# Kernel optimization log

Measured on AMD Instinct MI355X. Metric: run time of the kernel, lower is better.

The kernel has to match this reference:

```python
import jax, jax.numpy as jnp
import numpy as np

EPS = 1e-12

def setup_inputs() -> dict:
    key = jax.random.key(0)
    k1, k2, k3, k4, k5, k6 = jax.random.split(key, 6)
    B, DIM, T = 16, 256, 2048
    K, D = 1024, 64  # num_embeddings, embedding_dim
    N = B * T
    input_data = jax.random.normal(k1, (B, DIM, T), dtype=jnp.float32)
    codebooks = jax.random.normal(k2, (K, D), dtype=jnp.float32)
    W_in = jax.random.normal(k3, (DIM, D), dtype=jnp.float32) / np.sqrt(DIM)
    b_in = jnp.zeros((D,), dtype=jnp.float32)
    W_out = jax.random.normal(k4, (D, DIM), dtype=jnp.float32) / np.sqrt(D)
    b_out = jnp.zeros((DIM,), dtype=jnp.float32)
    random_vector = jax.random.normal(k5, (N, D), dtype=jnp.float32)
    return {"input_data": input_data, "codebooks": codebooks,
            "W_in": W_in, "b_in": b_in, "W_out": W_out, "b_out": b_out,
            "random_vector": random_vector}

def reference(input_data, codebooks, W_in, b_in, W_out, b_out, random_vector):
    B, DIM, T = input_data.shape
    D = codebooks.shape[1]
    # encode: [B, DIM, T] -> [B, T, DIM] -> project -> [B*T, D]
    x = jnp.einsum('bct,cd->btd', input_data, W_in) + b_in
    x = x.reshape(-1, D)  # [N, D]
    distances = (jnp.sum(x * x, axis=1, keepdims=True)
                 - 2.0 * (x @ codebooks.T)
                 + jnp.sum(codebooks * codebooks, axis=1)[None, :])  # [N, K]
    min_indices = jnp.argmin(distances, axis=1)  # [N]
    hard = codebooks[min_indices]  # [N, D]
    # noise substitution
    norm_resid = jnp.sqrt(jnp.sum((x - hard) ** 2, axis=1, keepdims=True))
    norm_rand = jnp.sqrt(jnp.sum(random_vector ** 2, axis=1, keepdims=True))
    vq_error = (norm_resid / (norm_rand + EPS)) * random_vector
    q = x + vq_error  # [N, D]
    # decode: [N, D] -> [B, T, D] -> project_out -> [B, DIM, T]
    q = q.reshape(B, T, D)
    out = jnp.einsum('btd,dc->bct', q, W_out) + b_out[None, :, None]
    return out
```

## Files before the change

kernel.cpp:

```cpp
#include <hip/hip_runtime.h>
#include <hip/hip_bf16.h>

typedef __bf16 bf16x8 __attribute__((ext_vector_type(8)));
typedef unsigned short u16x8 __attribute__((ext_vector_type(8)));
typedef unsigned short u16x4 __attribute__((ext_vector_type(4)));
typedef float f32x4 __attribute__((ext_vector_type(4)));
typedef unsigned short u16;

constexpr int DIMc = 256, Tt = 2048, Kk = 1024, Dd = 64;

#define WS_WINT 0
#define WS_CBX  18432
#define WS_WOX  116736

__device__ __forceinline__ u16 f2b(float f) {
  unsigned u = __float_as_uint(f);
  return (u16)((u + 0x7FFFu + ((u >> 16) & 1u)) >> 16);
}
__device__ __forceinline__ float b2f(u16 v) {
  return __uint_as_float(((unsigned)v) << 16);
}
__device__ __forceinline__ f32x4 mfma16(u16x8 a, u16x8 b, f32x4 c) {
  return __builtin_amdgcn_mfma_f32_16x16x32_bf16(
      __builtin_bit_cast(bf16x8, a), __builtin_bit_cast(bf16x8, b), c, 0, 0, 0);
}
__device__ __forceinline__ void dma16(const u16* g, u16* l) {
  __builtin_amdgcn_global_load_lds(
      (const __attribute__((address_space(1))) unsigned int*)g,
      (__attribute__((address_space(3))) unsigned int*)l, 16, 0, 0);
}

__global__ void nsvq_prep(const float* __restrict__ cb, const float* __restrict__ Win,
                          const float* __restrict__ bin, const float* __restrict__ Wout,
                          const float* __restrict__ bout, u16* __restrict__ wsu) {
  const int g = blockIdx.x * 256 + threadIdx.x;
  u16* WinT = wsu + WS_WINT;
  u16* CbX  = wsu + WS_CBX;
  u16* WoX  = wsu + WS_WOX;
  for (int i = g; i < 16384; i += 8192) {
    int c = i >> 6, d = i & 63;
    WinT[d * 288 + c] = f2b(Win[i]);
  }
  if (g < 2048) {
    int d = g >> 5, j = g & 31; u16 v = 0;
    float bv = bin[d]; u16 h = f2b(bv);
    if (j == 0) v = h; else if (j == 1) v = f2b(bv - b2f(h));
    WinT[d * 288 + 256 + j] = v;
  }
  if (g < 1024) {
    const float4* cr = (const float4*)(cb + (size_t)g * 64);
    float vb[64]; float cn = 0.f;
    #pragma unroll
    for (int q = 0; q < 16; ++q) {
      float4 v = cr[q];
      vb[q*4] = v.x; vb[q*4+1] = v.y; vb[q*4+2] = v.z; vb[q*4+3] = v.w;
      cn = fmaf(v.x, v.x, fmaf(v.y, v.y, fmaf(v.z, v.z, fmaf(v.w, v.w, cn))));
    }
    u16* row = CbX + g * 96;
    #pragma unroll
    for (int d = 0; d < 64; ++d) row[d] = f2b(-2.f * vb[d]);
    u16 h = f2b(cn);
    row[64] = h; row[65] = f2b(cn - b2f(h));
    for (int j = 66; j < 96; ++j) row[j] = 0;
  }
  for (int i = g; i < 16384; i += 8192) {
    int d = i >> 8, c = i & 255;
    WoX[c * 96 + d] = f2b(Wout[i]);
  }
  {
    int c = g >> 5, j = g & 31; u16 v = 0;
    float bv = bout[c]; u16 h = f2b(bv);
    if (j == 0) v = h; else if (j == 1) v = f2b(bv - b2f(h));
    WoX[c * 96 + 64 + j] = v;
  }
}

__global__ __launch_bounds__(512, 2) void nsvq_main(
    const float* __restrict__ in, const float* __restrict__ rnd,
    const u16* __restrict__ wsu, float* __restrict__ out) {
  __shared__ u16 buf[24576];
  __shared__ u16 InT[128 * 256];
  __shared__ u16 Xt[128 * 64];
  __shared__ float mnp[8][128];

  const int tid = threadIdx.x;
  const int lane = tid & 63;
  const int w = tid >> 6;
  const int quad = lane >> 4, col = lane & 15;
  const int b  = blockIdx.x >> 4;
  const int t0 = (blockIdx.x & 15) << 7;
  const int myt = w * 16 + col;

  {
    const int t = tid & 127, cg = tid >> 7;
    const float* ib = in + (size_t)b * DIMc * Tt + t0 + t;
    #pragma unroll
    for (int it = 0; it < 8; ++it) {
      int c0 = cg * 8 + it * 32;
      u16x8 pk;
      #pragma unroll
      for (int j = 0; j < 8; ++j) pk[j] = f2b(ib[(size_t)(c0 + j) * Tt]);
      *(u16x8*)(InT + t * 256 + ((((c0 >> 3)) ^ (t & 7)) << 3)) = pk;
    }
  }
  #pragma unroll
  for (int ii = 0; ii < 5; ++ii) {
    int i = w + 8 * ii;
    if (i < 36) dma16(wsu + WS_WINT + i * 512 + lane * 8, buf + i * 512);
  }
  float rr2v = 0.f;
  const float* rb = rnd + ((size_t)b * Tt + t0) * Dd;
  #pragma unroll
  for (int tt = 0; tt < 16; ++tt) {
    float v = rb[(size_t)(w * 16 + tt) * Dd + lane];
    float s = v * v;
    s += __shfl_xor(s, 1);  s += __shfl_xor(s, 2);  s += __shfl_xor(s, 4);
    s += __shfl_xor(s, 8);  s += __shfl_xor(s, 16); s += __shfl_xor(s, 32);
    if (col == tt) rr2v = s;
  }
  __syncthreads();

  u16x8 Bc1 = {0, 0, 0, 0, 0, 0, 0, 0};
  if (quad == 0) { Bc1[0] = 0x3F80; Bc1[1] = 0x3F80; }
  f32x4 acc[4];
  {
    u16x8 Bf[8];
    #pragma unroll
    for (int kt = 0; kt < 8; ++kt)
      Bf[kt] = *(const u16x8*)(InT + myt * 256 + (((kt * 4 + quad) ^ (myt & 7)) << 3));
    #pragma unroll
    for (int mt = 0; mt < 4; ++mt) {
      f32x4 a = {0.f, 0.f, 0.f, 0.f};
      #pragma unroll
      for (int kt = 0; kt < 8; ++kt) {
        u16x8 A = *(const u16x8*)(buf + (mt * 16 + col) * 288 + kt * 32 + quad * 8);
        a = mfma16(A, Bf[kt], a);
      }
      u16x8 A8 = *(const u16x8*)(buf + (mt * 16 + col) * 288 + 256 + quad * 8);
      acc[mt] = mfma16(A8, Bc1, a);
    }
  }
  float x2v = 0.f;
  #pragma unroll
  for (int mt = 0; mt < 4; ++mt) {
    u16x4 pk;
    #pragma unroll
    for (int r = 0; r < 4; ++r) { x2v = fmaf(acc[mt][r], acc[mt][r], x2v); pk[r] = f2b(acc[mt][r]); }
    int bk = mt * 2 + (quad >> 1);
    *(u16x4*)(Xt + myt * 64 + ((bk ^ (myt & 7)) << 3) + (quad & 1) * 4) = pk;
  }
  x2v += __shfl_xor(x2v, 16);
  x2v += __shfl_xor(x2v, 32);
  __syncthreads();

  u16x8 Xa[8], Xb[8];
  #pragma unroll
  for (int nt = 0; nt < 8; ++nt) {
    int tr = nt * 16 + col;
    Xa[nt] = *(const u16x8*)(Xt + tr * 64 + ((quad ^ (tr & 7)) << 3));
    Xb[nt] = *(const u16x8*)(Xt + tr * 64 + (((4 + quad) ^ (tr & 7)) << 3));
  }
  float minv[8];
  #pragma unroll
  for (int i = 0; i < 8; ++i) minv[i] = 3.4e38f;
  for (int ch = 0; ch < 4; ++ch) {
    if (ch) __syncthreads();
    #pragma unroll
    for (int ii = 0; ii < 6; ++ii) {
      int i = w + 8 * ii;
      dma16(wsu + WS_CBX + ch * 24576 + i * 512 + lane * 8, buf + i * 512);
    }
    __syncthreads();
    #pragma unroll
    for (int ms = 0; ms < 2; ++ms) {
      const u16* ar = buf + (w * 32 + ms * 16 + col) * 96;
      u16x8 A0 = *(const u16x8*)(ar + quad * 8);
      u16x8 A1 = *(const u16x8*)(ar + 32 + quad * 8);
      u16x8 A2 = *(const u16x8*)(ar + 64 + quad * 8);
      #pragma unroll
      for (int nt = 0; nt < 8; ++nt) {
        f32x4 a = {0.f, 0.f, 0.f, 0.f};
        a = mfma16(A0, Xa[nt], a);
        a = mfma16(A1, Xb[nt], a);
        a = mfma16(A2, Bc1, a);
        #pragma unroll
        for (int r = 0; r < 4; ++r) minv[nt] = fminf(minv[nt], a[r]);
      }
    }
  }
  #pragma unroll
  for (int nt = 0; nt < 8; ++nt) {
    float m = minv[nt];
    m = fminf(m, __shfl_xor(m, 16));
    m = fminf(m, __shfl_xor(m, 32));
    mnp[w][nt * 16 + col] = m;
  }
  __syncthreads();

  #pragma unroll
  for (int ii = 0; ii < 6; ++ii) {
    int i = w + 8 * ii;
    dma16(wsu + WS_WOX + i * 512 + lane * 8, buf + i * 512);
  }
  float mv = 3.4e38f;
  #pragma unroll
  for (int j = 0; j < 8; ++j) mv = fminf(mv, mnp[j][myt]);
  float r2  = fmaxf(x2v + mv, 0.f);
  float scv = sqrtf(r2) / (sqrtf(rr2v) + 1e-12f);
  #pragma unroll
  for (int tt = 0; tt < 16; ++tt) {
    float s = __shfl(scv, tt);
    float rv = rb[(size_t)(w * 16 + tt) * Dd + lane];
    int tr = w * 16 + tt;
    int idx = tr * 64 + (((lane >> 3) ^ (tr & 7)) << 3) + (lane & 7);
    Xt[idx] = f2b(fmaf(s, rv, b2f(Xt[idx])));
  }
  __syncthreads();

  u16x8 Q0 = *(const u16x8*)(Xt + myt * 64 + ((quad ^ (myt & 7)) << 3));
  u16x8 Q1 = *(const u16x8*)(Xt + myt * 64 + (((4 + quad) ^ (myt & 7)) << 3));
  float* ob0 = out + (size_t)b * DIMc * Tt + t0 + myt;
  #pragma unroll
  for (int mt = 0; mt < 16; ++mt) {
    const u16* ar = buf + (mt * 16 + col) * 96;
    u16x8 A0 = *(const u16x8*)(ar + quad * 8);
    u16x8 A1 = *(const u16x8*)(ar + 32 + quad * 8);
    u16x8 A2 = *(const u16x8*)(ar + 64 + quad * 8);
    f32x4 a = {0.f, 0.f, 0.f, 0.f};
    a = mfma16(A0, Q0, a);
    a = mfma16(A1, Q1, a);
    a = mfma16(A2, Bc1, a);
    float* ob = ob0 + (size_t)(mt * 16 + quad * 4) * Tt;
    #pragma unroll
    for (int r = 0; r < 4; ++r) ob[(size_t)r * Tt] = a[r];
  }
}

extern "C" void kernel_launch(void* const* d_in, const int* in_sizes, int n_in,
                              void* d_out, int out_size, void* d_ws, size_t ws_size,
                              hipStream_t stream) {
  const float *in = nullptr, *cb = nullptr, *rnd = nullptr, *bin = nullptr, *bout = nullptr;
  const float* w16[2] = {nullptr, nullptr}; int nw = 0;
  for (int i = 0; i < n_in; ++i) {
    switch (in_sizes[i]) {
      case 8388608: in  = (const float*)d_in[i]; break;
      case 65536:   cb  = (const float*)d_in[i]; break;
      case 2097152: rnd = (const float*)d_in[i]; break;
      case 64:      bin = (const float*)d_in[i]; break;
      case 256:     bout= (const float*)d_in[i]; break;
      case 16384:   if (nw < 2) w16[nw++] = (const float*)d_in[i]; break;
      default: break;
    }
  }
  if (!in)  in  = (const float*)d_in[0];
  if (!cb)  cb  = (const float*)d_in[1];
  if (nw < 2) { w16[0] = (const float*)d_in[2]; w16[1] = (const float*)d_in[4]; }
  if (!bin) bin = (const float*)d_in[3];
  if (!bout) bout = (const float*)d_in[5];
  if (!rnd) rnd = (const float*)d_in[6];

  u16* wsu = (u16*)d_ws;
  float* outp = (float*)d_out;

  nsvq_prep<<<32, 256, 0, stream>>>(cb, w16[0], bin, w16[1], bout, wsu);
  nsvq_main<<<256, 512, 0, stream>>>(in, rnd, wsu, outp);
}
```

Baseline: 116.3 us.

## Fuse weight prep into main kernel and stream codebook from global

Removes the separate prep kernel and workspace. Each block now converts W_in and W_out to bf16 into shared memory itself, and reads codebook rows straight from global memory into MFMA operands, computing the codebook norms on the fly. The -2 scale moves onto a second copy of x kept in shared memory. Biases and codebook norms are now fed as MFMA accumulator initial values instead of extra MFMAs with split bf16 hi/lo terms, which trades away that hi/lo precision trick. This saves one launch and the per-chunk LDS staging and barriers, at the cost of redundant weight conversion in every block, more global codebook traffic per block, and a larger shared-memory footprint.

```diff
diff --git a/kernel.cpp b/kernel.cpp
--- a/kernel.cpp
+++ b/kernel.cpp
@@ -3,15 +3,12 @@
 
 typedef __bf16 bf16x8 __attribute__((ext_vector_type(8)));
 typedef unsigned short u16x8 __attribute__((ext_vector_type(8)));
-typedef unsigned short u16x4 __attribute__((ext_vector_type(4)));
+typedef unsigned int u32x2 __attribute__((ext_vector_type(2)));
+typedef unsigned int u32x4 __attribute__((ext_vector_type(4)));
 typedef float f32x4 __attribute__((ext_vector_type(4)));
 typedef unsigned short u16;
 
-constexpr int DIMc = 256, Tt = 2048, Kk = 1024, Dd = 64;
-
-#define WS_WINT 0
-#define WS_CBX  18432
-#define WS_WOX  116736
+constexpr int DIMc = 256, Tt = 2048, Dd = 64;
 
 __device__ __forceinline__ u16 f2b(float f) {
   unsigned u = __float_as_uint(f);
@@ -20,93 +17,61 @@
 __device__ __forceinline__ float b2f(u16 v) {
   return __uint_as_float(((unsigned)v) << 16);
 }
+__device__ __forceinline__ unsigned f2b2(float a, float b) {
+  return (unsigned)f2b(a) | ((unsigned)f2b(b) << 16);
+}
 __device__ __forceinline__ f32x4 mfma16(u16x8 a, u16x8 b, f32x4 c) {
   return __builtin_amdgcn_mfma_f32_16x16x32_bf16(
       __builtin_bit_cast(bf16x8, a), __builtin_bit_cast(bf16x8, b), c, 0, 0, 0);
 }
-__device__ __forceinline__ void dma16(const u16* g, u16* l) {
-  __builtin_amdgcn_global_load_lds(
-      (const __attribute__((address_space(1))) unsigned int*)g,
-      (__attribute__((address_space(3))) unsigned int*)l, 16, 0, 0);
-}
-
-__global__ void nsvq_prep(const float* __restrict__ cb, const float* __restrict__ Win,
-                          const float* __restrict__ bin, const float* __restrict__ Wout,
-                          const float* __restrict__ bout, u16* __restrict__ wsu) {
-  const int g = blockIdx.x * 256 + threadIdx.x;
-  u16* WinT = wsu + WS_WINT;
-  u16* CbX  = wsu + WS_CBX;
-  u16* WoX  = wsu + WS_WOX;
-  for (int i = g; i < 16384; i += 8192) {
-    int c = i >> 6, d = i & 63;
-    WinT[d * 288 + c] = f2b(Win[i]);
-  }
-  if (g < 2048) {
-    int d = g >> 5, j = g & 31; u16 v = 0;
-    float bv = bin[d]; u16 h = f2b(bv);
-    if (j == 0) v = h; else if (j == 1) v = f2b(bv - b2f(h));
-    WinT[d * 288 + 256 + j] = v;
-  }
-  if (g < 1024) {
-    const float4* cr = (const float4*)(cb + (size_t)g * 64);
-    float vb[64]; float cn = 0.f;
-    #pragma unroll
-    for (int q = 0; q < 16; ++q) {
-      float4 v = cr[q];
-      vb[q*4] = v.x; vb[q*4+1] = v.y; vb[q*4+2] = v.z; vb[q*4+3] = v.w;
-      cn = fmaf(v.x, v.x, fmaf(v.y, v.y, fmaf(v.z, v.z, fmaf(v.w, v.w, cn))));
-    }
-    u16* row = CbX + g * 96;
-    #pragma unroll
-    for (int d = 0; d < 64; ++d) row[d] = f2b(-2.f * vb[d]);
-    u16 h = f2b(cn);
-    row[64] = h; row[65] = f2b(cn - b2f(h));
-    for (int j = 66; j < 96; ++j) row[j] = 0;
-  }
-  for (int i = g; i < 16384; i += 8192) {
-    int d = i >> 8, c = i & 255;
-    WoX[c * 96 + d] = f2b(Wout[i]);
-  }
-  {
-    int c = g >> 5, j = g & 31; u16 v = 0;
-    float bv = bout[c]; u16 h = f2b(bv);
-    if (j == 0) v = h; else if (j == 1) v = f2b(bv - b2f(h));
-    WoX[c * 96 + 64 + j] = v;
-  }
-}
-
-__global__ __launch_bounds__(512, 2) void nsvq_main(
+
+__global__ __launch_bounds__(512, 2) void nsvq_fused(
     const float* __restrict__ in, const float* __restrict__ rnd,
-    const u16* __restrict__ wsu, float* __restrict__ out) {
-  __shared__ u16 buf[24576];
-  __shared__ u16 InT[128 * 256];
-  __shared__ u16 Xt[128 * 64];
-  __shared__ float mnp[8][128];
-
-  const int tid = threadIdx.x;
+    const float* __restrict__ cb, const float* __restrict__ Win,
+    const float* __restrict__ bin, const float* __restrict__ Wout,
+    const float* __restrict__ bout, float* __restrict__ out) {
+  __shared__ u16 sm[69632];
+  u16* const WinT = sm;
+  u16* const InT  = sm + 18432;
+  u16* const WoX  = sm + 18432;
+  u16* const Xt   = sm + 51200;
+  u16* const Xm   = sm + 59392;
+  float* const mnp = (float*)(sm + 67584);
+
+  const int tid  = threadIdx.x;
   const int lane = tid & 63;
-  const int w = tid >> 6;
+  const int w    = tid >> 6;
   const int quad = lane >> 4, col = lane & 15;
-  const int b  = blockIdx.x >> 4;
-  const int t0 = (blockIdx.x & 15) << 7;
-  const int myt = w * 16 + col;
-
+  const int b    = blockIdx.x >> 4;
+  const int t0   = (blockIdx.x & 15) << 7;
+  const int myt  = w * 16 + col;
+
+  {
+    const int c = tid & 255, db = tid >> 8;
+    #pragma unroll
+    for (int k = 0; k < 4; ++k) {
+      const int d0 = db * 32 + k * 8;
+      const float4* wr = (const float4*)(Win + c * 64 + d0);
+      float4 v0 = wr[0], v1 = wr[1];
+      u16* dst = WinT + c;
+      dst[(d0 + 0) * 288] = f2b(v0.x); dst[(d0 + 1) * 288] = f2b(v0.y);
+      dst[(d0 + 2) * 288] = f2b(v0.z); dst[(d0 + 3) * 288] = f2b(v0.w);
+      dst[(d0 + 4) * 288] = f2b(v1.x); dst[(d0 + 5) * 288] = f2b(v1.y);
+      dst[(d0 + 6) * 288] = f2b(v1.z); dst[(d0 + 7) * 288] = f2b(v1.w);
+    }
+  }
   {
     const int t = tid & 127, cg = tid >> 7;
     const float* ib = in + (size_t)b * DIMc * Tt + t0 + t;
     #pragma unroll
     for (int it = 0; it < 8; ++it) {
-      int c0 = cg * 8 + it * 32;
-      u16x8 pk;
-      #pragma unroll
-      for (int j = 0; j < 8; ++j) pk[j] = f2b(ib[(size_t)(c0 + j) * Tt]);
-      *(u16x8*)(InT + t * 256 + ((((c0 >> 3)) ^ (t & 7)) << 3)) = pk;
-    }
-  }
-  #pragma unroll
-  for (int ii = 0; ii < 5; ++ii) {
-    int i = w + 8 * ii;
-    if (i < 36) dma16(wsu + WS_WINT + i * 512 + lane * 8, buf + i * 512);
+      const int c0 = cg * 8 + it * 32;
+      u32x4 pk;
+      #pragma unroll
+      for (int jj = 0; jj < 4; ++jj)
+        pk[jj] = f2b2(ib[(size_t)(c0 + 2 * jj) * Tt], ib[(size_t)(c0 + 2 * jj + 1) * Tt]);
+      *(u32x4*)(InT + t * 256 + (((c0 >> 3) ^ (t & 7)) << 3)) = pk;
+    }
   }
   float rr2v = 0.f;
   const float* rb = rnd + ((size_t)b * Tt + t0) * Dd;
@@ -120,8 +85,6 @@
   }
   __syncthreads();
 
-  u16x8 Bc1 = {0, 0, 0, 0, 0, 0, 0, 0};
-  if (quad == 0) { Bc1[0] = 0x3F80; Bc1[1] = 0x3F80; }
   f32x4 acc[4];
   {
     u16x8 Bf[8];
@@ -130,62 +93,80 @@
       Bf[kt] = *(const u16x8*)(InT + myt * 256 + (((kt * 4 + quad) ^ (myt & 7)) << 3));
     #pragma unroll
     for (int mt = 0; mt < 4; ++mt) {
-      f32x4 a = {0.f, 0.f, 0.f, 0.f};
+      float4 bi = *(const float4*)(bin + mt * 16 + quad * 4);
+      f32x4 a = {bi.x, bi.y, bi.z, bi.w};
       #pragma unroll
       for (int kt = 0; kt < 8; ++kt) {
-        u16x8 A = *(const u16x8*)(buf + (mt * 16 + col) * 288 + kt * 32 + quad * 8);
+        u16x8 A = *(const u16x8*)(WinT + (mt * 16 + col) * 288 + kt * 32 + quad * 8);
         a = mfma16(A, Bf[kt], a);
       }
-      u16x8 A8 = *(const u16x8*)(buf + (mt * 16 + col) * 288 + 256 + quad * 8);
-      acc[mt] = mfma16(A8, Bc1, a);
+      acc[mt] = a;
     }
   }
   float x2v = 0.f;
   #pragma unroll
   for (int mt = 0; mt < 4; ++mt) {
-    u16x4 pk;
-    #pragma unroll
-    for (int r = 0; r < 4; ++r) { x2v = fmaf(acc[mt][r], acc[mt][r], x2v); pk[r] = f2b(acc[mt][r]); }
-    int bk = mt * 2 + (quad >> 1);
-    *(u16x4*)(Xt + myt * 64 + ((bk ^ (myt & 7)) << 3) + (quad & 1) * 4) = pk;
+    #pragma unroll
+    for (int r = 0; r < 4; ++r) x2v = fmaf(acc[mt][r], acc[mt][r], x2v);
+    u32x2 px = { f2b2(acc[mt][0], acc[mt][1]), f2b2(acc[mt][2], acc[mt][3]) };
+    u32x2 pm = { f2b2(-2.f * acc[mt][0], -2.f * acc[mt][1]),
+                 f2b2(-2.f * acc[mt][2], -2.f * acc[mt][3]) };
+    const int bk  = mt * 2 + (quad >> 1);
+    const int off = myt * 64 + ((bk ^ (myt & 7)) << 3) + (quad & 1) * 4;
+    *(u32x2*)(Xt + off) = px;
+    *(u32x2*)(Xm + off) = pm;
   }
   x2v += __shfl_xor(x2v, 16);
   x2v += __shfl_xor(x2v, 32);
   __syncthreads();
 
+  {
+    const int c = tid & 255, db = tid >> 8;
+    #pragma unroll
+    for (int k = 0; k < 4; ++k) {
+      const int d0 = db * 32 + k * 8;
+      u32x4 pk;
+      #pragma unroll
+      for (int jj = 0; jj < 4; ++jj)
+        pk[jj] = f2b2(Wout[(size_t)(d0 + 2 * jj) * 256 + c],
+                      Wout[(size_t)(d0 + 2 * jj + 1) * 256 + c]);
+      *(u32x4*)(WoX + c * 72 + d0) = pk;
+    }
+  }
   u16x8 Xa[8], Xb[8];
   #pragma unroll
   for (int nt = 0; nt < 8; ++nt) {
-    int tr = nt * 16 + col;
-    Xa[nt] = *(const u16x8*)(Xt + tr * 64 + ((quad ^ (tr & 7)) << 3));
-    Xb[nt] = *(const u16x8*)(Xt + tr * 64 + (((4 + quad) ^ (tr & 7)) << 3));
+    const int tr = nt * 16 + col;
+    Xa[nt] = *(const u16x8*)(Xm + tr * 64 + ((quad ^ (tr & 7)) << 3));
+    Xb[nt] = *(const u16x8*)(Xm + tr * 64 + (((4 + quad) ^ (tr & 7)) << 3));
   }
   float minv[8];
   #pragma unroll
   for (int i = 0; i < 8; ++i) minv[i] = 3.4e38f;
-  for (int ch = 0; ch < 4; ++ch) {
-    if (ch) __syncthreads();
-    #pragma unroll
-    for (int ii = 0; ii < 6; ++ii) {
-      int i = w + 8 * ii;
-      dma16(wsu + WS_CBX + ch * 24576 + i * 512 + lane * 8, buf + i * 512);
-    }
-    __syncthreads();
-    #pragma unroll
-    for (int ms = 0; ms < 2; ++ms) {
-      const u16* ar = buf + (w * 32 + ms * 16 + col) * 96;
-      u16x8 A0 = *(const u16x8*)(ar + quad * 8);
-      u16x8 A1 = *(const u16x8*)(ar + 32 + quad * 8);
-      u16x8 A2 = *(const u16x8*)(ar + 64 + quad * 8);
-      #pragma unroll
-      for (int nt = 0; nt < 8; ++nt) {
-        f32x4 a = {0.f, 0.f, 0.f, 0.f};
-        a = mfma16(A0, Xa[nt], a);
-        a = mfma16(A1, Xb[nt], a);
-        a = mfma16(A2, Bc1, a);
-        #pragma unroll
-        for (int r = 0; r < 4; ++r) minv[nt] = fminf(minv[nt], a[r]);
-      }
+  const float* cw = cb + (size_t)(w * 128) * Dd;
+  for (int mi = 0; mi < 8; ++mi) {
+    const float* cr = cw + (size_t)(mi * 16 + col) * Dd + quad * 8;
+    float4 c0 = ((const float4*)cr)[0],        c1 = ((const float4*)cr)[1];
+    float4 c2 = ((const float4*)(cr + 32))[0], c3 = ((const float4*)(cr + 32))[1];
+    float cnA = fmaf(c0.w, c0.w, fmaf(c0.z, c0.z, fmaf(c0.y, c0.y, c0.x * c0.x)));
+    float cnB = fmaf(c1.w, c1.w, fmaf(c1.z, c1.z, fmaf(c1.y, c1.y, c1.x * c1.x)));
+    float cnC = fmaf(c2.w, c2.w, fmaf(c2.z, c2.z, fmaf(c2.y, c2.y, c2.x * c2.x)));
+    float cnD = fmaf(c3.w, c3.w, fmaf(c3.z, c3.z, fmaf(c3.y, c3.y, c3.x * c3.x)));
+    float cn = (cnA + cnB) + (cnC + cnD);
+    cn += __shfl_xor(cn, 16); cn += __shfl_xor(cn, 32);
+    f32x4 cn4;
+    #pragma unroll
+    for (int r = 0; r < 4; ++r) cn4[r] = __shfl(cn, quad * 4 + r);
+    u32x4 a0 = { f2b2(c0.x, c0.y), f2b2(c0.z, c0.w), f2b2(c1.x, c1.y), f2b2(c1.z, c1.w) };
+    u32x4 a1 = { f2b2(c2.x, c2.y), f2b2(c2.z, c2.w), f2b2(c3.x, c3.y), f2b2(c3.z, c3.w) };
+    u16x8 A0 = __builtin_bit_cast(u16x8, a0);
+    u16x8 A1 = __builtin_bit_cast(u16x8, a1);
+    #pragma unroll
+    for (int nt = 0; nt < 8; ++nt) {
+      f32x4 a = mfma16(A0, Xa[nt], cn4);
+      a = mfma16(A1, Xb[nt], a);
+      #pragma unroll
+      for (int r = 0; r < 4; ++r) minv[nt] = fminf(minv[nt], a[r]);
     }
   }
   #pragma unroll
@@ -193,43 +174,36 @@
     float m = minv[nt];
     m = fminf(m, __shfl_xor(m, 16));
     m = fminf(m, __shfl_xor(m, 32));
-    mnp[w][nt * 16 + col] = m;
+    mnp[w * 128 + nt * 16 + col] = m;
   }
   __syncthreads();
 
-  #pragma unroll
-  for (int ii = 0; ii < 6; ++ii) {
-    int i = w + 8 * ii;
-    dma16(wsu + WS_WOX + i * 512 + lane * 8, buf + i * 512);
-  }
   float mv = 3.4e38f;
   #pragma unroll
-  for (int j = 0; j < 8; ++j) mv = fminf(mv, mnp[j][myt]);
+  for (int j = 0; j < 8; ++j) mv = fminf(mv, mnp[j * 128 + myt]);
   float r2  = fmaxf(x2v + mv, 0.f);
   float scv = sqrtf(r2) / (sqrtf(rr2v) + 1e-12f);
   #pragma unroll
   for (int tt = 0; tt < 16; ++tt) {
-    float s = __shfl(scv, tt);
+    float s  = __shfl(scv, tt);
     float rv = rb[(size_t)(w * 16 + tt) * Dd + lane];
-    int tr = w * 16 + tt;
-    int idx = tr * 64 + (((lane >> 3) ^ (tr & 7)) << 3) + (lane & 7);
+    const int tr  = w * 16 + tt;
+    const int idx = tr * 64 + (((lane >> 3) ^ (tr & 7)) << 3) + (lane & 7);
     Xt[idx] = f2b(fmaf(s, rv, b2f(Xt[idx])));
   }
-  __syncthreads();
 
   u16x8 Q0 = *(const u16x8*)(Xt + myt * 64 + ((quad ^ (myt & 7)) << 3));
   u16x8 Q1 = *(const u16x8*)(Xt + myt * 64 + (((4 + quad) ^ (myt & 7)) << 3));
   float* ob0 = out + (size_t)b * DIMc * Tt + t0 + myt;
   #pragma unroll
   for (int mt = 0; mt < 16; ++mt) {
-    const u16* ar = buf + (mt * 16 + col) * 96;
+    const u16* ar = WoX + (mt * 16 + col) * 72;
     u16x8 A0 = *(const u16x8*)(ar + quad * 8);
     u16x8 A1 = *(const u16x8*)(ar + 32 + quad * 8);
-    u16x8 A2 = *(const u16x8*)(ar + 64 + quad * 8);
-    f32x4 a = {0.f, 0.f, 0.f, 0.f};
+    float4 bo = *(const float4*)(bout + mt * 16 + quad * 4);
+    f32x4 a = {bo.x, bo.y, bo.z, bo.w};
     a = mfma16(A0, Q0, a);
     a = mfma16(A1, Q1, a);
-    a = mfma16(A2, Bc1, a);
     float* ob = ob0 + (size_t)(mt * 16 + quad * 4) * Tt;
     #pragma unroll
     for (int r = 0; r < 4; ++r) ob[(size_t)r * Tt] = a[r];
@@ -239,12 +213,12 @@
 extern "C" void kernel_launch(void* const* d_in, const int* in_sizes, int n_in,
                               void* d_out, int out_size, void* d_ws, size_t ws_size,
                               hipStream_t stream) {
-  const float *in = nullptr, *cb = nullptr, *rnd = nullptr, *bin = nullptr, *bout = nullptr;
+  const float *in = nullptr, *cbp = nullptr, *rnd = nullptr, *bin = nullptr, *bout = nullptr;
   const float* w16[2] = {nullptr, nullptr}; int nw = 0;
   for (int i = 0; i < n_in; ++i) {
     switch (in_sizes[i]) {
       case 8388608: in  = (const float*)d_in[i]; break;
-      case 65536:   cb  = (const float*)d_in[i]; break;
+      case 65536:   cbp = (const float*)d_in[i]; break;
       case 2097152: rnd = (const float*)d_in[i]; break;
       case 64:      bin = (const float*)d_in[i]; break;
       case 256:     bout= (const float*)d_in[i]; break;
@@ -252,16 +226,12 @@
       default: break;
     }
   }
-  if (!in)  in  = (const float*)d_in[0];
-  if (!cb)  cb  = (const float*)d_in[1];
+  if (!in)   in  = (const float*)d_in[0];
+  if (!cbp)  cbp = (const float*)d_in[1];
   if (nw < 2) { w16[0] = (const float*)d_in[2]; w16[1] = (const float*)d_in[4]; }
-  if (!bin) bin = (const float*)d_in[3];
+  if (!bin)  bin = (const float*)d_in[3];
   if (!bout) bout = (const float*)d_in[5];
-  if (!rnd) rnd = (const float*)d_in[6];
-
-  u16* wsu = (u16*)d_ws;
-  float* outp = (float*)d_out;
-
-  nsvq_prep<<<32, 256, 0, stream>>>(cb, w16[0], bin, w16[1], bout, wsu);
-  nsvq_main<<<256, 512, 0, stream>>>(in, rnd, wsu, outp);
-}
+  if (!rnd)  rnd = (const float*)d_in[6];
+
+  nsvq_fused<<<256, 512, 0, stream>>>(in, rnd, cbp, w16[0], bin, w16[1], bout, (float*)d_out);
+}
```

Measured after the change: 112.4 us. 3.3% less time.
